# Performance work log

Measured on AMD Instinct MI355X. Metric: run time of the kernel, lower is better.

## Reference

```python
import jax, jax.numpy as jnp
import numpy as np

N_NODES = 1_000_000
MEM_DIM = 128
MSG_DIM = 256
N_UPD = 200_000


def setup_inputs() -> dict:
    key = jax.random.key(0)
    k0, k1, k2, k3, k4 = jax.random.split(key, 5)
    memory = jax.random.normal(k0, (N_NODES, MEM_DIM), dtype=jnp.float32)
    last_update = jnp.zeros((N_NODES,), dtype=jnp.float32)
    # 'unique' node ids: arange guarantees uniqueness and in-range values
    unique_node_ids = jnp.arange(N_UPD, dtype=jnp.int32)
    unique_messages = jax.random.normal(k1, (N_UPD, MSG_DIM), dtype=jnp.float32)
    timestamps = jax.random.uniform(k2, (N_UPD,), dtype=jnp.float32) * 1000.0
    # torch.nn.GRUCell parameters (the TGN memory_updater)
    scale = 1.0 / np.sqrt(MEM_DIM)
    W_ih = jax.random.uniform(k3, (3 * MEM_DIM, MSG_DIM), jnp.float32, -scale, scale)
    W_hh = jax.random.uniform(k4, (3 * MEM_DIM, MEM_DIM), jnp.float32, -scale, scale)
    b_ih = jnp.zeros((3 * MEM_DIM,), jnp.float32)
    b_hh = jnp.zeros((3 * MEM_DIM,), jnp.float32)
    return {
        "memory": memory,
        "last_update": last_update,
        "unique_node_ids": unique_node_ids,
        "unique_messages": unique_messages,
        "timestamps": timestamps,
        "W_ih": W_ih,
        "W_hh": W_hh,
        "b_ih": b_ih,
        "b_hh": b_hh,
    }


def _gru_cell(x, h, W_ih, W_hh, b_ih, b_hh):
    # torch.nn.GRUCell math
    gi = x @ W_ih.T + b_ih          # [U, 3H]
    gh = h @ W_hh.T + b_hh          # [U, 3H]
    i_r, i_z, i_n = jnp.split(gi, 3, axis=-1)
    h_r, h_z, h_n = jnp.split(gh, 3, axis=-1)
    r = jax.nn.sigmoid(i_r + h_r)
    z = jax.nn.sigmoid(i_z + h_z)
    n = jnp.tanh(i_n + r * h_n)
    return (1.0 - z) * n + z * h


def reference(memory, last_update, unique_node_ids, unique_messages, timestamps,
              W_ih, W_hh, b_ih, b_hh):
    # gather rows of the node memory (get_memory / updated_memory[unique_node_ids])
    h = memory[unique_node_ids]                              # [U, H]
    new_h = _gru_cell(unique_messages, h, W_ih, W_hh, b_ih, b_hh)
    # scatter updated rows back (set_memory) and update timestamps
    updated_memory = memory.at[unique_node_ids].set(new_h)
    updated_last_update = last_update.at[unique_node_ids].set(timestamps)
    return updated_memory, updated_last_update
```

## Files before the change

kernel.cpp:

```cpp
#include <hip/hip_runtime.h>
#include <hip/hip_bf16.h>
#include <stdint.h>

#define MEM_DIM 128
#define MSG_DIM 256
#define KTOT    384
#define BM      64

typedef __attribute__((ext_vector_type(8))) __bf16 bf16x8;
typedef __attribute__((ext_vector_type(4))) float  f32x4;

union B8u { uint32_t u[4]; bf16x8 v; };

__device__ __forceinline__ uint32_t cvt_pk(float lo, float hi) {
    uint32_t r;
    asm("v_cvt_pk_bf16_f32 %0, %1, %2" : "=v"(r) : "v"(lo), "v"(hi));
    return r;
}

__device__ __forceinline__ bf16x8 load_cvt8(const float* __restrict__ p) {
    f32x4 a = *(const f32x4*)p;
    f32x4 b = *(const f32x4*)(p + 4);
    B8u r;
    r.u[0] = cvt_pk(a.x, a.y);
    r.u[1] = cvt_pk(a.z, a.w);
    r.u[2] = cvt_pk(b.x, b.y);
    r.u[3] = cvt_pk(b.z, b.w);
    return r.v;
}

__device__ __forceinline__ float sigm(float x) {
    return __builtin_amdgcn_rcpf(1.0f + __expf(-x));
}
__device__ __forceinline__ float tanh_fast(float x) {
    return 1.0f - 2.0f * __builtin_amdgcn_rcpf(1.0f + __expf(2.0f * x));
}

__global__ void bm_zero_kernel(uint32_t* __restrict__ bm, int nwords) {
    int i = blockIdx.x * 256 + threadIdx.x;
    if (i < nwords) bm[i] = 0;
}
__global__ void bm_set_kernel(const int* __restrict__ ids, uint32_t* __restrict__ bm, int U) {
    int i = blockIdx.x * 256 + threadIdx.x;
    if (i < U) {
        int id = ids[i];
        atomicOr(&bm[id >> 5], 1u << (id & 31));
    }
}

__global__ void wconv_kernel(const float* __restrict__ wih,
                             const float* __restrict__ whh,
                             __hip_bfloat16* __restrict__ out) {
    int i = blockIdx.x * 256 + threadIdx.x;
    const int NIH = 3 * MEM_DIM * MSG_DIM;
    const int NHH = 3 * MEM_DIM * MEM_DIM;
    if (i < NIH)            out[i] = __float2bfloat16(wih[i]);
    else if (i < NIH + NHH) out[i] = __float2bfloat16(whh[i - NIH]);
}

__global__ void copy_skip_kernel(const f32x4* __restrict__ mem,
                                 const float* __restrict__ lu,
                                 f32x4* __restrict__ outm,
                                 float* __restrict__ outlu,
                                 const uint32_t* __restrict__ bm,
                                 int NN) {
    const int64_t n_mem_chunks = (int64_t)NN * 32;
    const int64_t total = n_mem_chunks + NN;
    const int64_t stride = (int64_t)gridDim.x * blockDim.x;
    for (int64_t i = (int64_t)blockIdx.x * blockDim.x + threadIdx.x; i < total; i += stride) {
        if (i < n_mem_chunks) {
            int row = (int)(i >> 5);
            if (!((bm[row >> 5] >> (row & 31)) & 1u)) {
                f32x4 v = __builtin_nontemporal_load(&mem[i]);
                __builtin_nontemporal_store(v, &outm[i]);
            }
        } else {
            int node = (int)(i - n_mem_chunks);
            if (!((bm[node >> 5] >> (node & 31)) & 1u))
                outlu[node] = lu[node];
        }
    }
}

__global__ void copy_all_kernel(const f32x4* __restrict__ mem,
                                const f32x4* __restrict__ lu,
                                f32x4* __restrict__ out,
                                int n_mem4, int n_tot4) {
    int stride = gridDim.x * blockDim.x;
    for (int i = blockIdx.x * blockDim.x + threadIdx.x; i < n_tot4; i += stride) {
        f32x4 v = (i < n_mem4) ? mem[i]
                               : __builtin_nontemporal_load(&lu[i - n_mem4]);
        __builtin_nontemporal_store(v, &out[i]);
    }
}

__device__ __forceinline__ int at_addr(int row, int kbyte) {
    return (row * (KTOT * 2) + kbyte) ^ ((row & 7) << 4);
}

template<bool PRE>
__global__ __launch_bounds__(512, 4)
void gru_stream_kernel(const float* __restrict__ memory,
                       const int*   __restrict__ ids,
                       const float* __restrict__ msgs,
                       const float* __restrict__ ts,
                       const float* __restrict__ Wih,
                       const float* __restrict__ Whh,
                       const float* __restrict__ bih,
                       const float* __restrict__ bhh,
                       const __hip_bfloat16* __restrict__ WihB,
                       const __hip_bfloat16* __restrict__ WhhB,
                       float* __restrict__ out_mem,
                       float* __restrict__ out_lu,
                       int U) {
    __shared__ __align__(16) char At[BM * KTOT * 2];

    const int tid  = threadIdx.x;
    const int w    = tid >> 6;
    const int lane = tid & 63;
    const int lq   = lane & 15;
    const int lk   = lane >> 4;
    const int rb   = blockIdx.x * BM;

    if (tid < BM) {
        int r = rb + tid;
        if (r < U) out_lu[ids[r]] = ts[r];
    }

    {
        int r = tid >> 3, seg = tid & 7;
        int rA = rb + r; if (rA >= U) rA = U - 1;
        const float* xp = msgs + (size_t)rA * MSG_DIM + seg * 32;
        #pragma unroll
        for (int i = 0; i < 4; ++i)
            *(bf16x8*)(At + at_addr(r, seg * 64 + i * 16)) = load_cvt8(xp + i * 8);
    }
    {
        int r = tid >> 3, u = tid & 7;
        int rA = rb + r; if (rA >= U) rA = U - 1;
        const float* hp = memory + (size_t)ids[rA] * MEM_DIM + u * 16;
        *(bf16x8*)(At + at_addr(r, 512 + u * 32))      = load_cvt8(hp);
        *(bf16x8*)(At + at_addr(r, 512 + u * 32 + 16)) = load_cvt8(hp + 8);
    }

    const int c = w * 16 + lq;
    const float br  = bih[c] + bhh[c];
    const float bz  = bih[MEM_DIM + c] + bhh[MEM_DIM + c];
    const float bin = bih[2 * MEM_DIM + c];
    const float bhn = bhh[2 * MEM_DIM + c];

    const __hip_bfloat16* wih_l = WihB + c * MSG_DIM + lk * 8;
    const __hip_bfloat16* whh_l = WhhB + c * MEM_DIM + lk * 8;
    const float* wih_f = Wih + c * MSG_DIM + lk * 8;
    const float* whh_f = Whh + c * MEM_DIM + lk * 8;

    const f32x4 z4 = {0.f, 0.f, 0.f, 0.f};
    f32x4 acc[4][4];
    #pragma unroll
    for (int m = 0; m < 4; ++m)
        #pragma unroll
        for (int q = 0; q < 4; ++q) acc[m][q] = z4;

    __syncthreads();

    #pragma unroll 1
    for (int ks = 0; ks < 8; ++ks) {
        bf16x8 bv0, bv1, bv2;
        if (PRE) {
            bv0 = *(const bf16x8*)(wih_l + 0 * 128 * MSG_DIM + ks * 32);
            bv1 = *(const bf16x8*)(wih_l + 1 * 128 * MSG_DIM + ks * 32);
            bv2 = *(const bf16x8*)(wih_l + 2 * 128 * MSG_DIM + ks * 32);
        } else {
            bv0 = load_cvt8(wih_f + 0 * 128 * MSG_DIM + ks * 32);
            bv1 = load_cvt8(wih_f + 1 * 128 * MSG_DIM + ks * 32);
            bv2 = load_cvt8(wih_f + 2 * 128 * MSG_DIM + ks * 32);
        }
        bf16x8 af[4];
        #pragma unroll
        for (int m = 0; m < 4; ++m)
            af[m] = *(const bf16x8*)(At + at_addr(m * 16 + lq, ks * 64 + lk * 16));
        #pragma unroll
        for (int m = 0; m < 4; ++m)
            acc[m][0] = __builtin_amdgcn_mfma_f32_16x16x32_bf16(af[m], bv0, acc[m][0], 0, 0, 0);
        #pragma unroll
        for (int m = 0; m < 4; ++m)
            acc[m][1] = __builtin_amdgcn_mfma_f32_16x16x32_bf16(af[m], bv1, acc[m][1], 0, 0, 0);
        #pragma unroll
        for (int m = 0; m < 4; ++m)
            acc[m][2] = __builtin_amdgcn_mfma_f32_16x16x32_bf16(af[m], bv2, acc[m][2], 0, 0, 0);
    }
    #pragma unroll 1
    for (int ks = 0; ks < 4; ++ks) {
        bf16x8 bv0, bv1, bv2;
        if (PRE) {
            bv0 = *(const bf16x8*)(whh_l + 0 * 128 * MEM_DIM + ks * 32);
            bv1 = *(const bf16x8*)(whh_l + 1 * 128 * MEM_DIM + ks * 32);
            bv2 = *(const bf16x8*)(whh_l + 2 * 128 * MEM_DIM + ks * 32);
        } else {
            bv0 = load_cvt8(whh_f + 0 * 128 * MEM_DIM + ks * 32);
            bv1 = load_cvt8(whh_f + 1 * 128 * MEM_DIM + ks * 32);
            bv2 = load_cvt8(whh_f + 2 * 128 * MEM_DIM + ks * 32);
        }
        bf16x8 af[4];
        #pragma unroll
        for (int m = 0; m < 4; ++m)
            af[m] = *(const bf16x8*)(At + at_addr(m * 16 + lq, 512 + ks * 64 + lk * 16));
        #pragma unroll
        for (int m = 0; m < 4; ++m)
            acc[m][0] = __builtin_amdgcn_mfma_f32_16x16x32_bf16(af[m], bv0, acc[m][0], 0, 0, 0);
        #pragma unroll
        for (int m = 0; m < 4; ++m)
            acc[m][1] = __builtin_amdgcn_mfma_f32_16x16x32_bf16(af[m], bv1, acc[m][1], 0, 0, 0);
        #pragma unroll
        for (int m = 0; m < 4; ++m)
            acc[m][3] = __builtin_amdgcn_mfma_f32_16x16x32_bf16(af[m], bv2, acc[m][3], 0, 0, 0);
    }

    #pragma unroll
    for (int m = 0; m < 4; ++m) {
        #pragma unroll
        for (int j = 0; j < 4; ++j) {
            int row = m * 16 + lk * 4 + j;
            int r = rb + row;
            if (r < U) {
                int id = ids[r];
                float hold = __bfloat162float(
                    *(const __hip_bfloat16*)(At + at_addr(row, 512 + c * 2)));
                float rg = sigm(acc[m][0][j] + br);
                float zg = sigm(acc[m][1][j] + bz);
                float ng = tanh_fast(acc[m][2][j] + bin + rg * (acc[m][3][j] + bhn));
                out_mem[(size_t)id * MEM_DIM + c] = (1.0f - zg) * ng + zg * hold;
            }
        }
    }
}

extern "C" void kernel_launch(void* const* d_in, const int* in_sizes, int n_in,
                              void* d_out, int out_size, void* d_ws, size_t ws_size,
                              hipStream_t stream) {
    const float* memory      = (const float*)d_in[0];
    const float* last_update = (const float*)d_in[1];
    const int*   ids         = (const int*)  d_in[2];
    const float* msgs        = (const float*)d_in[3];
    const float* ts          = (const float*)d_in[4];
    const float* Wih         = (const float*)d_in[5];
    const float* Whh         = (const float*)d_in[6];
    const float* bih         = (const float*)d_in[7];
    const float* bhh         = (const float*)d_in[8];

    const int NN = in_sizes[1];
    const int U  = in_sizes[2];

    float* out_mem = (float*)d_out;
    float* out_lu  = out_mem + (size_t)NN * MEM_DIM;

    const int NIH = 3 * MEM_DIM * MSG_DIM;
    const int NHH = 3 * MEM_DIM * MEM_DIM;
    const size_t WBYTES  = (size_t)(NIH + NHH) * sizeof(__hip_bfloat16);
    const size_t BM_OFF  = (WBYTES + 255) & ~(size_t)255;
    const int    BMWORDS = (NN + 31) / 32;
    const int    nblocks = (U + BM - 1) / BM;

    if (ws_size >= BM_OFF + (size_t)BMWORDS * 4) {
        __hip_bfloat16* wb = (__hip_bfloat16*)d_ws;
        uint32_t* bm = (uint32_t*)((char*)d_ws + BM_OFF);

        wconv_kernel<<<(NIH + NHH + 255) / 256, 256, 0, stream>>>(Wih, Whh, wb);
        bm_zero_kernel<<<(BMWORDS + 255) / 256, 256, 0, stream>>>(bm, BMWORDS);
        bm_set_kernel<<<(U + 255) / 256, 256, 0, stream>>>(ids, bm, U);

        gru_stream_kernel<true><<<nblocks, 512, 0, stream>>>(
            memory, ids, msgs, ts, Wih, Whh, bih, bhh,
            wb, wb + NIH, out_mem, out_lu, U);

        copy_skip_kernel<<<8192, 256, 0, stream>>>((const f32x4*)memory, last_update,
                                                   (f32x4*)out_mem, out_lu, bm, NN);
    } else {
        int n_mem4 = NN * MEM_DIM / 4;
        int n_tot4 = n_mem4 + NN / 4;
        copy_all_kernel<<<8192, 256, 0, stream>>>((const f32x4*)memory,
                                                  (const f32x4*)last_update,
                                                  (f32x4*)d_out, n_mem4, n_tot4);
        gru_stream_kernel<false><<<nblocks, 512, 0, stream>>>(
            memory, ids, msgs, ts, Wih, Whh, bih, bhh,
            nullptr, nullptr, out_mem, out_lu, U);
    }
}
```

Before: 353.4 us.

## Fuse GRU compute and skip-copy into one kernel with atomic work queue

Merges the GRU tile kernel and the bitmap-filtered memory copy into a single launch. Blocks are grouped in fours: three do a GRU tile and one starts copying right away, and every block then pulls copy batches from a global atomic counter until the arrays are covered. The aim is to overlap the compute-bound GRU with the bandwidth-bound copy and drop a separate kernel launch and its tail. The cost is an atomic per batch plus extra barriers. The fallback path passes the workspace as the counter with NN=0, which may be unsafe if the workspace is too small.

After: 411.0 us. 16.3% more time.

```diff
diff --git a/kernel.cpp b/kernel.cpp
--- a/kernel.cpp
+++ b/kernel.cpp
@@ -58,30 +58,6 @@
     else if (i < NIH + NHH) out[i] = __float2bfloat16(whh[i - NIH]);
 }
 
-__global__ void copy_skip_kernel(const f32x4* __restrict__ mem,
-                                 const float* __restrict__ lu,
-                                 f32x4* __restrict__ outm,
-                                 float* __restrict__ outlu,
-                                 const uint32_t* __restrict__ bm,
-                                 int NN) {
-    const int64_t n_mem_chunks = (int64_t)NN * 32;
-    const int64_t total = n_mem_chunks + NN;
-    const int64_t stride = (int64_t)gridDim.x * blockDim.x;
-    for (int64_t i = (int64_t)blockIdx.x * blockDim.x + threadIdx.x; i < total; i += stride) {
-        if (i < n_mem_chunks) {
-            int row = (int)(i >> 5);
-            if (!((bm[row >> 5] >> (row & 31)) & 1u)) {
-                f32x4 v = __builtin_nontemporal_load(&mem[i]);
-                __builtin_nontemporal_store(v, &outm[i]);
-            }
-        } else {
-            int node = (int)(i - n_mem_chunks);
-            if (!((bm[node >> 5] >> (node & 31)) & 1u))
-                outlu[node] = lu[node];
-        }
-    }
-}
-
 __global__ void copy_all_kernel(const f32x4* __restrict__ mem,
                                 const f32x4* __restrict__ lu,
                                 f32x4* __restrict__ out,
@@ -98,138 +74,183 @@
     return (row * (KTOT * 2) + kbyte) ^ ((row & 7) << 4);
 }
 
+#define BATCH_CHUNKS (512 * 16)
+
 template<bool PRE>
 __global__ __launch_bounds__(512, 4)
-void gru_stream_kernel(const float* __restrict__ memory,
-                       const int*   __restrict__ ids,
-                       const float* __restrict__ msgs,
-                       const float* __restrict__ ts,
-                       const float* __restrict__ Wih,
-                       const float* __restrict__ Whh,
-                       const float* __restrict__ bih,
-                       const float* __restrict__ bhh,
-                       const __hip_bfloat16* __restrict__ WihB,
-                       const __hip_bfloat16* __restrict__ WhhB,
-                       float* __restrict__ out_mem,
-                       float* __restrict__ out_lu,
-                       int U) {
+void gru_copy_kernel(const float* __restrict__ memory,
+                     const int*   __restrict__ ids,
+                     const float* __restrict__ msgs,
+                     const float* __restrict__ ts,
+                     const float* __restrict__ Wih,
+                     const float* __restrict__ Whh,
+                     const float* __restrict__ bih,
+                     const float* __restrict__ bhh,
+                     const __hip_bfloat16* __restrict__ WihB,
+                     const __hip_bfloat16* __restrict__ WhhB,
+                     const uint32_t* __restrict__ bm,
+                     uint32_t* __restrict__ ctr,
+                     const float* __restrict__ last_update,
+                     float* __restrict__ out_mem,
+                     float* __restrict__ out_lu,
+                     int U, int ntiles, int NN) {
     __shared__ __align__(16) char At[BM * KTOT * 2];
+    __shared__ uint32_t sbatch;
 
     const int tid  = threadIdx.x;
-    const int w    = tid >> 6;
-    const int lane = tid & 63;
-    const int lq   = lane & 15;
-    const int lk   = lane >> 4;
-    const int rb   = blockIdx.x * BM;
-
-    if (tid < BM) {
-        int r = rb + tid;
-        if (r < U) out_lu[ids[r]] = ts[r];
-    }
-
-    {
-        int r = tid >> 3, seg = tid & 7;
-        int rA = rb + r; if (rA >= U) rA = U - 1;
-        const float* xp = msgs + (size_t)rA * MSG_DIM + seg * 32;
-        #pragma unroll
-        for (int i = 0; i < 4; ++i)
-            *(bf16x8*)(At + at_addr(r, seg * 64 + i * 16)) = load_cvt8(xp + i * 8);
-    }
-    {
-        int r = tid >> 3, u = tid & 7;
-        int rA = rb + r; if (rA >= U) rA = U - 1;
-        const float* hp = memory + (size_t)ids[rA] * MEM_DIM + u * 16;
-        *(bf16x8*)(At + at_addr(r, 512 + u * 32))      = load_cvt8(hp);
-        *(bf16x8*)(At + at_addr(r, 512 + u * 32 + 16)) = load_cvt8(hp + 8);
-    }
-
-    const int c = w * 16 + lq;
-    const float br  = bih[c] + bhh[c];
-    const float bz  = bih[MEM_DIM + c] + bhh[MEM_DIM + c];
-    const float bin = bih[2 * MEM_DIM + c];
-    const float bhn = bhh[2 * MEM_DIM + c];
-
-    const __hip_bfloat16* wih_l = WihB + c * MSG_DIM + lk * 8;
-    const __hip_bfloat16* whh_l = WhhB + c * MEM_DIM + lk * 8;
-    const float* wih_f = Wih + c * MSG_DIM + lk * 8;
-    const float* whh_f = Whh + c * MEM_DIM + lk * 8;
-
-    const f32x4 z4 = {0.f, 0.f, 0.f, 0.f};
-    f32x4 acc[4][4];
-    #pragma unroll
-    for (int m = 0; m < 4; ++m)
-        #pragma unroll
-        for (int q = 0; q < 4; ++q) acc[m][q] = z4;
-
-    __syncthreads();
-
-    #pragma unroll 1
-    for (int ks = 0; ks < 8; ++ks) {
-        bf16x8 bv0, bv1, bv2;
-        if (PRE) {
-            bv0 = *(const bf16x8*)(wih_l + 0 * 128 * MSG_DIM + ks * 32);
-            bv1 = *(const bf16x8*)(wih_l + 1 * 128 * MSG_DIM + ks * 32);
-            bv2 = *(const bf16x8*)(wih_l + 2 * 128 * MSG_DIM + ks * 32);
-        } else {
-            bv0 = load_cvt8(wih_f + 0 * 128 * MSG_DIM + ks * 32);
-            bv1 = load_cvt8(wih_f + 1 * 128 * MSG_DIM + ks * 32);
-            bv2 = load_cvt8(wih_f + 2 * 128 * MSG_DIM + ks * 32);
-        }
-        bf16x8 af[4];
+    const int bid  = blockIdx.x;
+    const int grp  = bid >> 2, role = bid & 3;
+    const int t    = grp * 3 + role;
+
+    if (role != 3 && t < ntiles) {
+        const int w    = tid >> 6;
+        const int lane = tid & 63;
+        const int lq   = lane & 15;
+        const int lk   = lane >> 4;
+        const int rb   = t * BM;
+
+        if (tid < BM) {
+            int r = rb + tid;
+            if (r < U) out_lu[ids[r]] = ts[r];
+        }
+        {
+            int r = tid >> 3, seg = tid & 7;
+            int rA = rb + r; if (rA >= U) rA = U - 1;
+            const float* xp = msgs + (size_t)rA * MSG_DIM + seg * 32;
+            #pragma unroll
+            for (int i = 0; i < 4; ++i)
+                *(bf16x8*)(At + at_addr(r, seg * 64 + i * 16)) = load_cvt8(xp + i * 8);
+        }
+        {
+            int r = tid >> 3, u = tid & 7;
+            int rA = rb + r; if (rA >= U) rA = U - 1;
+            const float* hp = memory + (size_t)ids[rA] * MEM_DIM + u * 16;
+            *(bf16x8*)(At + at_addr(r, 512 + u * 32))      = load_cvt8(hp);
+            *(bf16x8*)(At + at_addr(r, 512 + u * 32 + 16)) = load_cvt8(hp + 8);
+        }
+
+        const int c = w * 16 + lq;
+        const float br  = bih[c] + bhh[c];
+        const float bz  = bih[MEM_DIM + c] + bhh[MEM_DIM + c];
+        const float bin = bih[2 * MEM_DIM + c];
+        const float bhn = bhh[2 * MEM_DIM + c];
+
+        const __hip_bfloat16* wih_l = WihB + c * MSG_DIM + lk * 8;
+        const __hip_bfloat16* whh_l = WhhB + c * MEM_DIM + lk * 8;
+        const float* wih_f = Wih + c * MSG_DIM + lk * 8;
+        const float* whh_f = Whh + c * MEM_DIM + lk * 8;
+
+        const f32x4 z4 = {0.f, 0.f, 0.f, 0.f};
+        f32x4 acc[4][4];
         #pragma unroll
         for (int m = 0; m < 4; ++m)
-            af[m] = *(const bf16x8*)(At + at_addr(m * 16 + lq, ks * 64 + lk * 16));
+            #pragma unroll
+            for (int q = 0; q < 4; ++q) acc[m][q] = z4;
+
+        __syncthreads();
+
+        #pragma unroll 1
+        for (int ks = 0; ks < 8; ++ks) {
+            bf16x8 bv0, bv1, bv2;
+            if (PRE) {
+                bv0 = *(const bf16x8*)(wih_l + 0 * 128 * MSG_DIM + ks * 32);
+                bv1 = *(const bf16x8*)(wih_l + 1 * 128 * MSG_DIM + ks * 32);
+                bv2 = *(const bf16x8*)(wih_l + 2 * 128 * MSG_DIM + ks * 32);
+            } else {
+                bv0 = load_cvt8(wih_f + 0 * 128 * MSG_DIM + ks * 32);
+                bv1 = load_cvt8(wih_f + 1 * 128 * MSG_DIM + ks * 32);
+                bv2 = load_cvt8(wih_f + 2 * 128 * MSG_DIM + ks * 32);
+            }
+            bf16x8 af[4];
+            #pragma unroll
+            for (int m = 0; m < 4; ++m)
+                af[m] = *(const bf16x8*)(At + at_addr(m * 16 + lq, ks * 64 + lk * 16));
+            #pragma unroll
+            for (int m = 0; m < 4; ++m)
+                acc[m][0] = __builtin_amdgcn_mfma_f32_16x16x32_bf16(af[m], bv0, acc[m][0], 0, 0, 0);
+            #pragma unroll
+            for (int m = 0; m < 4; ++m)
+                acc[m][1] = __builtin_amdgcn_mfma_f32_16x16x32_bf16(af[m], bv1, acc[m][1], 0, 0, 0);
+            #pragma unroll
+            for (int m = 0; m < 4; ++m)
+                acc[m][2] = __builtin_amdgcn_mfma_f32_16x16x32_bf16(af[m], bv2, acc[m][2], 0, 0, 0);
+        }
+        #pragma unroll 1
+        for (int ks = 0; ks < 4; ++ks) {
+            bf16x8 bv0, bv1, bv2;
+            if (PRE) {
+                bv0 = *(const bf16x8*)(whh_l + 0 * 128 * MEM_DIM + ks * 32);
+                bv1 = *(const bf16x8*)(whh_l + 1 * 128 * MEM_DIM + ks * 32);
+                bv2 = *(const bf16x8*)(whh_l + 2 * 128 * MEM_DIM + ks * 32);
+            } else {
+                bv0 = load_cvt8(whh_f + 0 * 128 * MEM_DIM + ks * 32);
+                bv1 = load_cvt8(whh_f + 1 * 128 * MEM_DIM + ks * 32);
+                bv2 = load_cvt8(whh_f + 2 * 128 * MEM_DIM + ks * 32);
+            }
+            bf16x8 af[4];
+            #pragma unroll
+            for (int m = 0; m < 4; ++m)
+                af[m] = *(const bf16x8*)(At + at_addr(m * 16 + lq, 512 + ks * 64 + lk * 16));
+            #pragma unroll
+            for (int m = 0; m < 4; ++m)
+                acc[m][0] = __builtin_amdgcn_mfma_f32_16x16x32_bf16(af[m], bv0, acc[m][0], 0, 0, 0);
+            #pragma unroll
+            for (int m = 0; m < 4; ++m)
+                acc[m][1] = __builtin_amdgcn_mfma_f32_16x16x32_bf16(af[m], bv1, acc[m][1], 0, 0, 0);
+            #pragma unroll
+            for (int m = 0; m < 4; ++m)
+                acc[m][3] = __builtin_amdgcn_mfma_f32_16x16x32_bf16(af[m], bv2, acc[m][3], 0, 0, 0);
+        }
+
         #pragma unroll
-        for (int m = 0; m < 4; ++m)
-            acc[m][0] = __builtin_amdgcn_mfma_f32_16x16x32_bf16(af[m], bv0, acc[m][0], 0, 0, 0);
+        for (int m = 0; m < 4; ++m) {
+            #pragma unroll
+            for (int j = 0; j < 4; ++j) {
+                int row = m * 16 + lk * 4 + j;
+                int r = rb + row;
+                if (r < U) {
+                    int id = ids[r];
+                    float hold = __bfloat162float(
+                        *(const __hip_bfloat16*)(At + at_addr(row, 512 + c * 2)));
+                    float rg = sigm(acc[m][0][j] + br);
+                    float zg = sigm(acc[m][1][j] + bz);
+                    float ng = tanh_fast(acc[m][2][j] + bin + rg * (acc[m][3][j] + bhn));
+                    __builtin_nontemporal_store((1.0f - zg) * ng + zg * hold,
+                                                &out_mem[(size_t)id * MEM_DIM + c]);
+                }
+            }
+        }
+    }
+
+    const int64_t n_mem_chunks = (int64_t)NN * 32;
+    const int64_t n_lu_chunks  = (NN + 3) >> 2;
+    const int64_t total_chunks = n_mem_chunks + n_lu_chunks;
+    const f32x4* memv = (const f32x4*)memory;
+    f32x4* outv = (f32x4*)out_mem;
+
+    for (;;) {
+        __syncthreads();
+        if (tid == 0) sbatch = atomicAdd(ctr, 1u);
+        __syncthreads();
+        int64_t base = (int64_t)sbatch * BATCH_CHUNKS;
+        if (base >= total_chunks) break;
         #pragma unroll
-        for (int m = 0; m < 4; ++m)
-            acc[m][1] = __builtin_amdgcn_mfma_f32_16x16x32_bf16(af[m], bv1, acc[m][1], 0, 0, 0);
-        #pragma unroll
-        for (int m = 0; m < 4; ++m)
-            acc[m][2] = __builtin_amdgcn_mfma_f32_16x16x32_bf16(af[m], bv2, acc[m][2], 0, 0, 0);
-    }
-    #pragma unroll 1
-    for (int ks = 0; ks < 4; ++ks) {
-        bf16x8 bv0, bv1, bv2;
-        if (PRE) {
-            bv0 = *(const bf16x8*)(whh_l + 0 * 128 * MEM_DIM + ks * 32);
-            bv1 = *(const bf16x8*)(whh_l + 1 * 128 * MEM_DIM + ks * 32);
-            bv2 = *(const bf16x8*)(whh_l + 2 * 128 * MEM_DIM + ks * 32);
-        } else {
-            bv0 = load_cvt8(whh_f + 0 * 128 * MEM_DIM + ks * 32);
-            bv1 = load_cvt8(whh_f + 1 * 128 * MEM_DIM + ks * 32);
-            bv2 = load_cvt8(whh_f + 2 * 128 * MEM_DIM + ks * 32);
-        }
-        bf16x8 af[4];
-        #pragma unroll
-        for (int m = 0; m < 4; ++m)
-            af[m] = *(const bf16x8*)(At + at_addr(m * 16 + lq, 512 + ks * 64 + lk * 16));
-        #pragma unroll
-        for (int m = 0; m < 4; ++m)
-            acc[m][0] = __builtin_amdgcn_mfma_f32_16x16x32_bf16(af[m], bv0, acc[m][0], 0, 0, 0);
-        #pragma unroll
-        for (int m = 0; m < 4; ++m)
-            acc[m][1] = __builtin_amdgcn_mfma_f32_16x16x32_bf16(af[m], bv1, acc[m][1], 0, 0, 0);
-        #pragma unroll
-        for (int m = 0; m < 4; ++m)
-            acc[m][3] = __builtin_amdgcn_mfma_f32_16x16x32_bf16(af[m], bv2, acc[m][3], 0, 0, 0);
-    }
-
-    #pragma unroll
-    for (int m = 0; m < 4; ++m) {
-        #pragma unroll
-        for (int j = 0; j < 4; ++j) {
-            int row = m * 16 + lk * 4 + j;
-            int r = rb + row;
-            if (r < U) {
-                int id = ids[r];
-                float hold = __bfloat162float(
-                    *(const __hip_bfloat16*)(At + at_addr(row, 512 + c * 2)));
-                float rg = sigm(acc[m][0][j] + br);
-                float zg = sigm(acc[m][1][j] + bz);
-                float ng = tanh_fast(acc[m][2][j] + bin + rg * (acc[m][3][j] + bhn));
-                out_mem[(size_t)id * MEM_DIM + c] = (1.0f - zg) * ng + zg * hold;
+        for (int k = 0; k < 16; ++k) {
+            int64_t i = base + k * 512 + tid;
+            if (i < n_mem_chunks) {
+                int row = (int)(i >> 5);
+                if (!((bm[row >> 5] >> (row & 31)) & 1u)) {
+                    f32x4 v = __builtin_nontemporal_load(&memv[i]);
+                    __builtin_nontemporal_store(v, &outv[i]);
+                }
+            } else if (i < total_chunks) {
+                int node = (int)(i - n_mem_chunks) * 4;
+                #pragma unroll
+                for (int j = 0; j < 4; ++j) {
+                    int n = node + j;
+                    if (n < NN && !((bm[n >> 5] >> (n & 31)) & 1u))
+                        out_lu[n] = last_update[n];
+                }
             }
         }
     }
@@ -259,30 +280,31 @@
     const size_t WBYTES  = (size_t)(NIH + NHH) * sizeof(__hip_bfloat16);
     const size_t BM_OFF  = (WBYTES + 255) & ~(size_t)255;
     const int    BMWORDS = (NN + 31) / 32;
-    const int    nblocks = (U + BM - 1) / BM;
-
-    if (ws_size >= BM_OFF + (size_t)BMWORDS * 4) {
+    const int    ntiles  = (U + BM - 1) / BM;
+    const int    ngrp    = (ntiles + 2) / 3;
+    const int    GRID    = ngrp * 4;
+
+    if (ws_size >= BM_OFF + (size_t)(BMWORDS + 1) * 4) {
         __hip_bfloat16* wb = (__hip_bfloat16*)d_ws;
-        uint32_t* bm = (uint32_t*)((char*)d_ws + BM_OFF);
+        uint32_t* bm  = (uint32_t*)((char*)d_ws + BM_OFF);
+        uint32_t* ctr = bm + BMWORDS;
 
         wconv_kernel<<<(NIH + NHH + 255) / 256, 256, 0, stream>>>(Wih, Whh, wb);
-        bm_zero_kernel<<<(BMWORDS + 255) / 256, 256, 0, stream>>>(bm, BMWORDS);
+        bm_zero_kernel<<<(BMWORDS + 1 + 255) / 256, 256, 0, stream>>>(bm, BMWORDS + 1);
         bm_set_kernel<<<(U + 255) / 256, 256, 0, stream>>>(ids, bm, U);
 
-        gru_stream_kernel<true><<<nblocks, 512, 0, stream>>>(
+        gru_copy_kernel<true><<<GRID, 512, 0, stream>>>(
             memory, ids, msgs, ts, Wih, Whh, bih, bhh,
-            wb, wb + NIH, out_mem, out_lu, U);
-
-        copy_skip_kernel<<<8192, 256, 0, stream>>>((const f32x4*)memory, last_update,
-                                                   (f32x4*)out_mem, out_lu, bm, NN);
+            wb, wb + NIH, bm, ctr, last_update, out_mem, out_lu, U, ntiles, NN);
     } else {
         int n_mem4 = NN * MEM_DIM / 4;
         int n_tot4 = n_mem4 + NN / 4;
         copy_all_kernel<<<8192, 256, 0, stream>>>((const f32x4*)memory,
                                                   (const f32x4*)last_update,
                                                   (f32x4*)d_out, n_mem4, n_tot4);
-        gru_stream_kernel<false><<<nblocks, 512, 0, stream>>>(
+        gru_copy_kernel<false><<<((U + BM - 1) / BM + 2) / 3 * 4, 512, 0, stream>>>(
             memory, ids, msgs, ts, Wih, Whh, bih, bhh,
-            nullptr, nullptr, out_mem, out_lu, U);
-    }
-}
+            nullptr, nullptr, nullptr, (uint32_t*)d_ws, last_update,
+            out_mem, out_lu, U, (U + BM - 1) / BM, 0);
+    }
+}
```

## Fuse skip-copy of untouched rows into GRU kernel to overlap with MFMA

Applied to the files above, without the earlier changes.

Removes the separate copy_skip kernel and distributes the bitmap-masked copy of non-updated memory rows and timestamps across the GRU blocks. Each block copies a contiguous slice of chunks, interleaving one copy step per K-iteration of the MFMA loop and finishing the rest after the epilogue. The aim is to hide the bandwidth-bound copy behind the compute-bound GEMM and save one launch. In exchange, each block now carries a large copy tail (about 130 KB of chunks with ~3125 blocks), and the 4-wide last_update tail is handled with scalar stores.

New measurement: 426.7 us. +20.8%, slower.

```diff
diff --git a/kernel.cpp b/kernel.cpp
--- a/kernel.cpp
+++ b/kernel.cpp
@@ -58,30 +58,6 @@
     else if (i < NIH + NHH) out[i] = __float2bfloat16(whh[i - NIH]);
 }
 
-__global__ void copy_skip_kernel(const f32x4* __restrict__ mem,
-                                 const float* __restrict__ lu,
-                                 f32x4* __restrict__ outm,
-                                 float* __restrict__ outlu,
-                                 const uint32_t* __restrict__ bm,
-                                 int NN) {
-    const int64_t n_mem_chunks = (int64_t)NN * 32;
-    const int64_t total = n_mem_chunks + NN;
-    const int64_t stride = (int64_t)gridDim.x * blockDim.x;
-    for (int64_t i = (int64_t)blockIdx.x * blockDim.x + threadIdx.x; i < total; i += stride) {
-        if (i < n_mem_chunks) {
-            int row = (int)(i >> 5);
-            if (!((bm[row >> 5] >> (row & 31)) & 1u)) {
-                f32x4 v = __builtin_nontemporal_load(&mem[i]);
-                __builtin_nontemporal_store(v, &outm[i]);
-            }
-        } else {
-            int node = (int)(i - n_mem_chunks);
-            if (!((bm[node >> 5] >> (node & 31)) & 1u))
-                outlu[node] = lu[node];
-        }
-    }
-}
-
 __global__ void copy_all_kernel(const f32x4* __restrict__ mem,
                                 const f32x4* __restrict__ lu,
                                 f32x4* __restrict__ out,
@@ -98,21 +74,23 @@
     return (row * (KTOT * 2) + kbyte) ^ ((row & 7) << 4);
 }
 
-template<bool PRE>
+template<bool PRE, bool COPY>
 __global__ __launch_bounds__(512, 4)
-void gru_stream_kernel(const float* __restrict__ memory,
-                       const int*   __restrict__ ids,
-                       const float* __restrict__ msgs,
-                       const float* __restrict__ ts,
-                       const float* __restrict__ Wih,
-                       const float* __restrict__ Whh,
-                       const float* __restrict__ bih,
-                       const float* __restrict__ bhh,
-                       const __hip_bfloat16* __restrict__ WihB,
-                       const __hip_bfloat16* __restrict__ WhhB,
-                       float* __restrict__ out_mem,
-                       float* __restrict__ out_lu,
-                       int U) {
+void gru_fused_kernel(const float* __restrict__ memory,
+                      const int*   __restrict__ ids,
+                      const float* __restrict__ msgs,
+                      const float* __restrict__ ts,
+                      const float* __restrict__ Wih,
+                      const float* __restrict__ Whh,
+                      const float* __restrict__ bih,
+                      const float* __restrict__ bhh,
+                      const __hip_bfloat16* __restrict__ WihB,
+                      const __hip_bfloat16* __restrict__ WhhB,
+                      const uint32_t* __restrict__ bm,
+                      const float* __restrict__ last_update,
+                      float* __restrict__ out_mem,
+                      float* __restrict__ out_lu,
+                      int U, int NN, int cpb) {
     __shared__ __align__(16) char At[BM * KTOT * 2];
 
     const int tid  = threadIdx.x;
@@ -122,6 +100,33 @@
     const int lk   = lane >> 4;
     const int rb   = blockIdx.x * BM;
 
+    const int64_t n_mem_chunks = (int64_t)NN * 32;
+    const int64_t total_chunks = n_mem_chunks + ((NN + 3) >> 2);
+    const int64_t cbase = (int64_t)blockIdx.x * cpb + tid;
+    const f32x4* memv = (const f32x4*)memory;
+    f32x4* outv = (f32x4*)out_mem;
+
+    auto copy_step = [&](int off) {
+        if (!COPY) return;
+        if (off >= cpb) return;
+        int64_t i = cbase + off;
+        if (i < n_mem_chunks) {
+            int row = (int)(i >> 5);
+            if (!((bm[row >> 5] >> (row & 31)) & 1u)) {
+                f32x4 v = __builtin_nontemporal_load(&memv[i]);
+                __builtin_nontemporal_store(v, &outv[i]);
+            }
+        } else if (i < total_chunks) {
+            int node = (int)(i - n_mem_chunks) * 4;
+            #pragma unroll
+            for (int j = 0; j < 4; ++j) {
+                int n = node + j;
+                if (n < NN && !((bm[n >> 5] >> (n & 31)) & 1u))
+                    out_lu[n] = last_update[n];
+            }
+        }
+    };
+
     if (tid < BM) {
         int r = rb + tid;
         if (r < U) out_lu[ids[r]] = ts[r];
@@ -165,6 +170,7 @@
 
     #pragma unroll 1
     for (int ks = 0; ks < 8; ++ks) {
+        copy_step(ks * 512);
         bf16x8 bv0, bv1, bv2;
         if (PRE) {
             bv0 = *(const bf16x8*)(wih_l + 0 * 128 * MSG_DIM + ks * 32);
@@ -191,6 +197,7 @@
     }
     #pragma unroll 1
     for (int ks = 0; ks < 4; ++ks) {
+        copy_step((8 + ks) * 512);
         bf16x8 bv0, bv1, bv2;
         if (PRE) {
             bv0 = *(const bf16x8*)(whh_l + 0 * 128 * MEM_DIM + ks * 32);
@@ -233,6 +240,12 @@
             }
         }
     }
+
+    if (COPY) {
+        #pragma unroll 1
+        for (int off = 12 * 512; off < cpb; off += 512)
+            copy_step(off);
+    }
 }
 
 extern "C" void kernel_launch(void* const* d_in, const int* in_sizes, int n_in,
@@ -261,6 +274,9 @@
     const int    BMWORDS = (NN + 31) / 32;
     const int    nblocks = (U + BM - 1) / BM;
 
+    const int64_t total_chunks = (int64_t)NN * 32 + ((NN + 3) >> 2);
+    const int     cpb = (int)((total_chunks + nblocks - 1) / nblocks);
+
     if (ws_size >= BM_OFF + (size_t)BMWORDS * 4) {
         __hip_bfloat16* wb = (__hip_bfloat16*)d_ws;
         uint32_t* bm = (uint32_t*)((char*)d_ws + BM_OFF);
@@ -269,20 +285,17 @@
         bm_zero_kernel<<<(BMWORDS + 255) / 256, 256, 0, stream>>>(bm, BMWORDS);
         bm_set_kernel<<<(U + 255) / 256, 256, 0, stream>>>(ids, bm, U);
 
-        gru_stream_kernel<true><<<nblocks, 512, 0, stream>>>(
+        gru_fused_kernel<true, true><<<nblocks, 512, 0, stream>>>(
             memory, ids, msgs, ts, Wih, Whh, bih, bhh,
-            wb, wb + NIH, out_mem, out_lu, U);
-
-        copy_skip_kernel<<<8192, 256, 0, stream>>>((const f32x4*)memory, last_update,
-                                                   (f32x4*)out_mem, out_lu, bm, NN);
+            wb, wb + NIH, bm, last_update, out_mem, out_lu, U, NN, cpb);
     } else {
         int n_mem4 = NN * MEM_DIM / 4;
         int n_tot4 = n_mem4 + NN / 4;
         copy_all_kernel<<<8192, 256, 0, stream>>>((const f32x4*)memory,
                                                   (const f32x4*)last_update,
                                                   (f32x4*)d_out, n_mem4, n_tot4);
-        gru_stream_kernel<false><<<nblocks, 512, 0, stream>>>(
+        gru_fused_kernel<false, false><<<nblocks, 512, 0, stream>>>(
             memory, ids, msgs, ts, Wih, Whh, bih, bhh,
-            nullptr, nullptr, out_mem, out_lu, U);
-    }
-}
+            nullptr, nullptr, nullptr, last_update, out_mem, out_lu, U, NN, 0);
+    }
+}
```

## Halve GRU row tile, reload fp32 old state, fuse init kernels, nontemporal I/O

Applied to the files above, without the earlier changes.

Shrinks the GRU block tile from 64 to 32 rows, so there are twice as many blocks and each holds less shared memory and fewer accumulator registers. The launch-bounds occupancy hint is dropped. The old hidden state used in the final blend is now read back as fp32 from global memory instead of the bf16 copy in LDS, and the nontemporal hints are added to message loads and output stores. The weight conversion and bitmap zeroing kernels are merged into a single init kernel to save a launch. In exchange, each weight fragment is reused across half as many rows, so weight traffic per row doubles.

Result: slower. 451.1 us (+27.6%).

```diff
diff --git a/kernel.cpp b/kernel.cpp
--- a/kernel.cpp
+++ b/kernel.cpp
@@ -5,7 +5,7 @@
 #define MEM_DIM 128
 #define MSG_DIM 256
 #define KTOT    384
-#define BM      64
+#define BM      32
 
 typedef __attribute__((ext_vector_type(8))) __bf16 bf16x8;
 typedef __attribute__((ext_vector_type(4))) float  f32x4;
@@ -29,6 +29,17 @@
     return r.v;
 }
 
+__device__ __forceinline__ bf16x8 load_cvt8_nt(const float* __restrict__ p) {
+    f32x4 a = __builtin_nontemporal_load((const f32x4*)p);
+    f32x4 b = __builtin_nontemporal_load((const f32x4*)(p + 4));
+    B8u r;
+    r.u[0] = cvt_pk(a.x, a.y);
+    r.u[1] = cvt_pk(a.z, a.w);
+    r.u[2] = cvt_pk(b.x, b.y);
+    r.u[3] = cvt_pk(b.z, b.w);
+    return r.v;
+}
+
 __device__ __forceinline__ float sigm(float x) {
     return __builtin_amdgcn_rcpf(1.0f + __expf(-x));
 }
@@ -36,9 +47,16 @@
     return 1.0f - 2.0f * __builtin_amdgcn_rcpf(1.0f + __expf(2.0f * x));
 }
 
-__global__ void bm_zero_kernel(uint32_t* __restrict__ bm, int nwords) {
+__global__ void init_kernel(const float* __restrict__ wih,
+                            const float* __restrict__ whh,
+                            __hip_bfloat16* __restrict__ wb,
+                            uint32_t* __restrict__ bm, int bmwords) {
     int i = blockIdx.x * 256 + threadIdx.x;
-    if (i < nwords) bm[i] = 0;
+    const int NIH = 3 * MEM_DIM * MSG_DIM;
+    const int NHH = 3 * MEM_DIM * MEM_DIM;
+    if (i < NIH)            wb[i] = __float2bfloat16(wih[i]);
+    else if (i < NIH + NHH) wb[i] = __float2bfloat16(whh[i - NIH]);
+    if (i < bmwords) bm[i] = 0;
 }
 __global__ void bm_set_kernel(const int* __restrict__ ids, uint32_t* __restrict__ bm, int U) {
     int i = blockIdx.x * 256 + threadIdx.x;
@@ -46,16 +64,6 @@
         int id = ids[i];
         atomicOr(&bm[id >> 5], 1u << (id & 31));
     }
-}
-
-__global__ void wconv_kernel(const float* __restrict__ wih,
-                             const float* __restrict__ whh,
-                             __hip_bfloat16* __restrict__ out) {
-    int i = blockIdx.x * 256 + threadIdx.x;
-    const int NIH = 3 * MEM_DIM * MSG_DIM;
-    const int NHH = 3 * MEM_DIM * MEM_DIM;
-    if (i < NIH)            out[i] = __float2bfloat16(wih[i]);
-    else if (i < NIH + NHH) out[i] = __float2bfloat16(whh[i - NIH]);
 }
 
 __global__ void copy_skip_kernel(const f32x4* __restrict__ mem,
@@ -99,20 +107,20 @@
 }
 
 template<bool PRE>
-__global__ __launch_bounds__(512, 4)
-void gru_stream_kernel(const float* __restrict__ memory,
-                       const int*   __restrict__ ids,
-                       const float* __restrict__ msgs,
-                       const float* __restrict__ ts,
-                       const float* __restrict__ Wih,
-                       const float* __restrict__ Whh,
-                       const float* __restrict__ bih,
-                       const float* __restrict__ bhh,
-                       const __hip_bfloat16* __restrict__ WihB,
-                       const __hip_bfloat16* __restrict__ WhhB,
-                       float* __restrict__ out_mem,
-                       float* __restrict__ out_lu,
-                       int U) {
+__global__ __launch_bounds__(512)
+void gru32_kernel(const float* __restrict__ memory,
+                  const int*   __restrict__ ids,
+                  const float* __restrict__ msgs,
+                  const float* __restrict__ ts,
+                  const float* __restrict__ Wih,
+                  const float* __restrict__ Whh,
+                  const float* __restrict__ bih,
+                  const float* __restrict__ bhh,
+                  const __hip_bfloat16* __restrict__ WihB,
+                  const __hip_bfloat16* __restrict__ WhhB,
+                  float* __restrict__ out_mem,
+                  float* __restrict__ out_lu,
+                  int U) {
     __shared__ __align__(16) char At[BM * KTOT * 2];
 
     const int tid  = threadIdx.x;
@@ -128,19 +136,17 @@
     }
 
     {
-        int r = tid >> 3, seg = tid & 7;
+        int r = tid >> 4, seg = tid & 15;
         int rA = rb + r; if (rA >= U) rA = U - 1;
-        const float* xp = msgs + (size_t)rA * MSG_DIM + seg * 32;
-        #pragma unroll
-        for (int i = 0; i < 4; ++i)
-            *(bf16x8*)(At + at_addr(r, seg * 64 + i * 16)) = load_cvt8(xp + i * 8);
+        const float* xp = msgs + (size_t)rA * MSG_DIM + seg * 16;
+        *(bf16x8*)(At + at_addr(r, seg * 32))      = load_cvt8_nt(xp);
+        *(bf16x8*)(At + at_addr(r, seg * 32 + 16)) = load_cvt8_nt(xp + 8);
     }
     {
-        int r = tid >> 3, u = tid & 7;
+        int r = tid >> 4, u = tid & 15;
         int rA = rb + r; if (rA >= U) rA = U - 1;
-        const float* hp = memory + (size_t)ids[rA] * MEM_DIM + u * 16;
-        *(bf16x8*)(At + at_addr(r, 512 + u * 32))      = load_cvt8(hp);
-        *(bf16x8*)(At + at_addr(r, 512 + u * 32 + 16)) = load_cvt8(hp + 8);
+        const float* hp = memory + (size_t)ids[rA] * MEM_DIM + u * 8;
+        *(bf16x8*)(At + at_addr(r, 512 + u * 16)) = load_cvt8(hp);
     }
 
     const int c = w * 16 + lq;
@@ -155,13 +161,24 @@
     const float* whh_f = Whh + c * MEM_DIM + lk * 8;
 
     const f32x4 z4 = {0.f, 0.f, 0.f, 0.f};
-    f32x4 acc[4][4];
+    f32x4 acc[2][4];
     #pragma unroll
-    for (int m = 0; m < 4; ++m)
+    for (int m = 0; m < 2; ++m)
         #pragma unroll
         for (int q = 0; q < 4; ++q) acc[m][q] = z4;
 
     __syncthreads();
+
+    int   oid[2][4];
+    float hv[2][4];
+    #pragma unroll
+    for (int m = 0; m < 2; ++m)
+        #pragma unroll
+        for (int j = 0; j < 4; ++j) {
+            int r = rb + m * 16 + lk * 4 + j;
+            oid[m][j] = ids[(r < U) ? r : (U - 1)];
+            hv[m][j]  = memory[(size_t)oid[m][j] * MEM_DIM + c];
+        }
 
     #pragma unroll 1
     for (int ks = 0; ks < 8; ++ks) {
@@ -175,18 +192,18 @@
             bv1 = load_cvt8(wih_f + 1 * 128 * MSG_DIM + ks * 32);
             bv2 = load_cvt8(wih_f + 2 * 128 * MSG_DIM + ks * 32);
         }
-        bf16x8 af[4];
-        #pragma unroll
-        for (int m = 0; m < 4; ++m)
+        bf16x8 af[2];
+        #pragma unroll
+        for (int m = 0; m < 2; ++m)
             af[m] = *(const bf16x8*)(At + at_addr(m * 16 + lq, ks * 64 + lk * 16));
         #pragma unroll
-        for (int m = 0; m < 4; ++m)
+        for (int m = 0; m < 2; ++m)
             acc[m][0] = __builtin_amdgcn_mfma_f32_16x16x32_bf16(af[m], bv0, acc[m][0], 0, 0, 0);
         #pragma unroll
-        for (int m = 0; m < 4; ++m)
+        for (int m = 0; m < 2; ++m)
             acc[m][1] = __builtin_amdgcn_mfma_f32_16x16x32_bf16(af[m], bv1, acc[m][1], 0, 0, 0);
         #pragma unroll
-        for (int m = 0; m < 4; ++m)
+        for (int m = 0; m < 2; ++m)
             acc[m][2] = __builtin_amdgcn_mfma_f32_16x16x32_bf16(af[m], bv2, acc[m][2], 0, 0, 0);
     }
     #pragma unroll 1
@@ -201,35 +218,33 @@
             bv1 = load_cvt8(whh_f + 1 * 128 * MEM_DIM + ks * 32);
             bv2 = load_cvt8(whh_f + 2 * 128 * MEM_DIM + ks * 32);
         }
-        bf16x8 af[4];
-        #pragma unroll
-        for (int m = 0; m < 4; ++m)
+        bf16x8 af[2];
+        #pragma unroll
+        for (int m = 0; m < 2; ++m)
             af[m] = *(const bf16x8*)(At + at_addr(m * 16 + lq, 512 + ks * 64 + lk * 16));
         #pragma unroll
-        for (int m = 0; m < 4; ++m)
+        for (int m = 0; m < 2; ++m)
             acc[m][0] = __builtin_amdgcn_mfma_f32_16x16x32_bf16(af[m], bv0, acc[m][0], 0, 0, 0);
         #pragma unroll
-        for (int m = 0; m < 4; ++m)
+        for (int m = 0; m < 2; ++m)
             acc[m][1] = __builtin_amdgcn_mfma_f32_16x16x32_bf16(af[m], bv1, acc[m][1], 0, 0, 0);
         #pragma unroll
-        for (int m = 0; m < 4; ++m)
+        for (int m = 0; m < 2; ++m)
             acc[m][3] = __builtin_amdgcn_mfma_f32_16x16x32_bf16(af[m], bv2, acc[m][3], 0, 0, 0);
     }
 
     #pragma unroll
-    for (int m = 0; m < 4; ++m) {
+    for (int m = 0; m < 2; ++m) {
         #pragma unroll
         for (int j = 0; j < 4; ++j) {
-            int row = m * 16 + lk * 4 + j;
-            int r = rb + row;
+            int r = rb + m * 16 + lk * 4 + j;
             if (r < U) {
-                int id = ids[r];
-                float hold = __bfloat162float(
-                    *(const __hip_bfloat16*)(At + at_addr(row, 512 + c * 2)));
                 float rg = sigm(acc[m][0][j] + br);
                 float zg = sigm(acc[m][1][j] + bz);
                 float ng = tanh_fast(acc[m][2][j] + bin + rg * (acc[m][3][j] + bhn));
-                out_mem[(size_t)id * MEM_DIM + c] = (1.0f - zg) * ng + zg * hold;
+                __builtin_nontemporal_store(
+                    (1.0f - zg) * ng + zg * hv[m][j],
+                    &out_mem[(size_t)oid[m][j] * MEM_DIM + c]);
             }
         }
     }
@@ -265,11 +280,11 @@
         __hip_bfloat16* wb = (__hip_bfloat16*)d_ws;
         uint32_t* bm = (uint32_t*)((char*)d_ws + BM_OFF);
 
-        wconv_kernel<<<(NIH + NHH + 255) / 256, 256, 0, stream>>>(Wih, Whh, wb);
-        bm_zero_kernel<<<(BMWORDS + 255) / 256, 256, 0, stream>>>(bm, BMWORDS);
+        int initn = (NIH + NHH > BMWORDS) ? (NIH + NHH) : BMWORDS;
+        init_kernel<<<(initn + 255) / 256, 256, 0, stream>>>(Wih, Whh, wb, bm, BMWORDS);
         bm_set_kernel<<<(U + 255) / 256, 256, 0, stream>>>(ids, bm, U);
 
-        gru_stream_kernel<true><<<nblocks, 512, 0, stream>>>(
+        gru32_kernel<true><<<nblocks, 512, 0, stream>>>(
             memory, ids, msgs, ts, Wih, Whh, bih, bhh,
             wb, wb + NIH, out_mem, out_lu, U);
 
@@ -281,7 +296,7 @@
         copy_all_kernel<<<8192, 256, 0, stream>>>((const f32x4*)memory,
                                                   (const f32x4*)last_update,
                                                   (f32x4*)d_out, n_mem4, n_tot4);
-        gru_stream_kernel<false><<<nblocks, 512, 0, stream>>>(
+        gru32_kernel<false><<<nblocks, 512, 0, stream>>>(
             memory, ids, msgs, ts, Wih, Whh, bih, bhh,
             nullptr, nullptr, out_mem, out_lu, U);
     }
```
